# Performance work log

Measured on AMD Instinct MI355X. Metric: run time of the kernel, lower is better.

The kernel has to match this reference:

```python
import jax, jax.numpy as jnp
import numpy as np

B, S, E, H = 2, 2048, 1024, 8
DH = E // H


def setup_inputs() -> dict:
    key = jax.random.key(0)
    ks = jax.random.split(key, 8)
    sc = 1.0 / np.sqrt(E)
    return {
        "q": jax.random.normal(ks[0], (B, S, E), jnp.float32),
        "k": jax.random.normal(ks[1], (B, S, E), jnp.float32),
        "v": jax.random.normal(ks[2], (B, S, E), jnp.float32),
        "Wq": jax.random.normal(ks[3], (E, E), jnp.float32) * sc,
        "bq": jnp.zeros((E,), jnp.float32),
        "Wk": jax.random.normal(ks[4], (E, E), jnp.float32) * sc,
        "bk": jnp.zeros((E,), jnp.float32),
        "Wv": jax.random.normal(ks[5], (E, E), jnp.float32) * sc,
        "bv": jnp.zeros((E,), jnp.float32),
        "Wo": jax.random.normal(ks[6], (E, E), jnp.float32) * sc,
        "bo": jnp.zeros((E,), jnp.float32),
        "is_causal": 1,
    }


def reference(q, k, v, Wq, bq, Wk, bk, Wv, bv, Wo, bo, is_causal):
    # q,k,v: [B,S,E]. Dense projections, split into H heads of dim DH.
    def heads(x, W, b):
        y = x @ W + b                       # [B,S,E]
        return y.reshape(B, S, H, DH).transpose(0, 2, 1, 3)  # [B,H,S,DH]

    qh = heads(q, Wq, bq)
    kh = heads(k, Wk, bk)
    vh = heads(v, Wv, bv)

    scale = 1.0 / jnp.sqrt(jnp.asarray(DH, q.dtype))
    scores = jnp.einsum("bhsd,bhtd->bhst", qh, kh) * scale  # [B,H,S,S]

    if is_causal:
        # tril mask (BigBird layout is all-ones here; causality comes from attn_mask)
        causal = jnp.tril(jnp.ones((S, S), bool))
        neg = jnp.asarray(jnp.finfo(scores.dtype).min, scores.dtype)
        scores = jnp.where(causal[None, None], scores, neg)

    attn = jax.nn.softmax(scores, axis=-1)                  # [B,H,S,S]
    ctx = jnp.einsum("bhst,bhtd->bhsd", attn, vh)           # [B,H,S,DH]
    ctx = ctx.transpose(0, 2, 1, 3).reshape(B, S, E)        # merge heads
    return ctx @ Wo + bo
```

## Files before the change

### kernel.cpp

```cpp
#include <hip/hip_runtime.h>
#include <math.h>


typedef __bf16 bf16_t;
typedef __bf16 bf16x8 __attribute__((ext_vector_type(8)));
typedef float f32x4 __attribute__((ext_vector_type(4)));

#define MFMA16(a, b, c) __builtin_amdgcn_mfma_f32_16x16x32_bf16(a, b, c, 0, 0, 0)

__global__ __launch_bounds__(256) void prep(const float* q, const float* k,
                                            const float* v, bf16_t* qb,
                                            bf16_t* kb, bf16_t* vb,
                                            const float* W0, const float* W1,
                                            const float* W2, const float* W3,
                                            bf16_t* Wt) {
  const int bid = blockIdx.x, tid = threadIdx.x;
  if (bid < 6144) {
    const int z = bid >> 11, chunk = bid & 2047;
    const float* x = (z == 0) ? q : (z == 1) ? k : v;
    bf16_t* y = (z == 0) ? qb : (z == 1) ? kb : vb;
    size_t i = ((size_t)chunk * 256 + tid) * 8;
    float4 a = *(const float4*)(x + i);
    float4 b = *(const float4*)(x + i + 4);
    bf16x8 o = {(bf16_t)a.x, (bf16_t)a.y, (bf16_t)a.z, (bf16_t)a.w,
                (bf16_t)b.x, (bf16_t)b.y, (bf16_t)b.z, (bf16_t)b.w};
    *(bf16x8*)(y + i) = o;
  } else {
    __shared__ float t[32][33];
    const int b2 = bid - 6144;
    const int wz = b2 >> 10, t2 = b2 & 1023;
    const float* W = (wz == 0) ? W0 : (wz == 1) ? W1 : (wz == 2) ? W2 : W3;
    bf16_t* o = Wt + (size_t)wz * 1024 * 1024;
    const int n0 = (t2 & 31) * 32, k0 = (t2 >> 5) * 32;
    const int tx = tid & 31, ty = tid >> 5;
#pragma unroll
    for (int i = 0; i < 4; i++)
      t[ty + 8 * i][tx] = W[(size_t)(k0 + ty + 8 * i) * 1024 + n0 + tx];
    __syncthreads();
#pragma unroll
    for (int i = 0; i < 4; i++)
      o[(size_t)(n0 + ty + 8 * i) * 1024 + k0 + tx] = (bf16_t)t[tx][ty + 8 * i];
  }
}

__global__ __launch_bounds__(256) void gemm_qkv(
    const bf16_t* qb, const bf16_t* kb, const bf16_t* vb, const bf16_t* Wt,
    const float* b0, const float* b1, const float* b2, bf16_t* Qh, bf16_t* Kh,
    bf16_t* Vt) {
  __shared__ bf16_t As[2][128 * 64];
  __shared__ bf16_t Bs[2][128 * 64];
  const int tid = threadIdx.x, w = tid >> 6, lane = tid & 63;
  const int bm = blockIdx.x, bn = blockIdx.y;
  const int wr = w >> 1, wc = w & 1, q4 = lane >> 4, lo = lane & 15;
  const int z = blockIdx.z;
  const bf16_t* A = (z == 0) ? qb : (z == 1) ? kb : vb;
  const bf16_t* Bt = Wt + (size_t)z * 1024 * 1024;
  const float* bias = (z == 0) ? b0 : (z == 1) ? b1 : b2;

  f32x4 acc[4][4];
#pragma unroll
  for (int m = 0; m < 4; m++)
#pragma unroll
    for (int n = 0; n < 4; n++) acc[m][n] = (f32x4){0.f, 0.f, 0.f, 0.f};

  const int r2 = tid >> 1;
  const int cb = (tid & 1) * 4;
  const bf16_t* Arow = A + (size_t)(bm * 128 + r2) * 1024;
  const bf16_t* Brow = Bt + (size_t)(bn * 128 + r2) * 1024;

  bf16x8 ar[4], br[4];
  auto loadAB = [&](int k0) {
#pragma unroll
    for (int i = 0; i < 4; i++) {
      ar[i] = *(const bf16x8*)(Arow + k0 + (cb + i) * 8);
      br[i] = *(const bf16x8*)(Brow + k0 + (cb + i) * 8);
    }
  };

  loadAB(0);
  for (int k = 0; k < 16; k++) {
    const int cur = k & 1;
#pragma unroll
    for (int i = 0; i < 4; i++) {
      *(bf16x8*)&As[cur][r2 * 64 + (((cb + i) ^ (r2 & 7)) * 8)] = ar[i];
      *(bf16x8*)&Bs[cur][r2 * 64 + (((cb + i) ^ (r2 & 7)) * 8)] = br[i];
    }
    if (k < 15) loadAB((k + 1) * 64);
    __syncthreads();

#pragma unroll
    for (int kc = 0; kc < 2; kc++) {
      bf16x8 af[4], bfr[4];
#pragma unroll
      for (int m = 0; m < 4; m++) {
        int rr = wr * 64 + m * 16 + lo;
        af[m] = *(const bf16x8*)&As[cur][rr * 64 + (((kc * 4 + q4) ^ (rr & 7)) * 8)];
      }
#pragma unroll
      for (int n = 0; n < 4; n++) {
        int rr = wc * 64 + n * 16 + lo;
        bfr[n] = *(const bf16x8*)&Bs[cur][rr * 64 + (((kc * 4 + q4) ^ (rr & 7)) * 8)];
      }
#pragma unroll
      for (int m = 0; m < 4; m++)
#pragma unroll
        for (int n = 0; n < 4; n++)
          acc[m][n] = MFMA16(af[m], bfr[n], acc[m][n]);
    }
  }

#pragma unroll
  for (int m = 0; m < 4; m++) {
#pragma unroll
    for (int n = 0; n < 4; n++) {
      int rowg0 = bm * 128 + wr * 64 + m * 16 + q4 * 4;
      int colg = bn * 128 + wc * 64 + n * 16 + lo;
      float bv = bias[colg];
#pragma unroll
      for (int rg = 0; rg < 4; rg++) {
        float val = acc[m][n][rg] + bv;
        int row = rowg0 + rg;
        int b = row >> 11, s = row & 2047;
        int h = colg >> 7, d = colg & 127;
        if (z == 0)
          Qh[(((size_t)(b * 8 + h)) * 2048 + s) * 128 + d] = (bf16_t)val;
        else if (z == 1)
          Kh[(((size_t)(b * 8 + h)) * 2048 + s) * 128 + d] = (bf16_t)val;
        else
          Vt[(((size_t)(b * 8 + h)) * 128 + d) * 2048 + s] = (bf16_t)val;
      }
    }
  }
}

__global__ __launch_bounds__(256) void gemm_out(const bf16_t* ctx,
                                                const bf16_t* Wt3,
                                                const float* bo, float* Of32) {
  __shared__ bf16_t As[2][64 * 64];
  __shared__ bf16_t Bs[2][128 * 64];
  const int tid = threadIdx.x, w = tid >> 6, lane = tid & 63;
  const int bm = blockIdx.x, bn = blockIdx.y;
  const int wr = w >> 1, wc = w & 1, q4 = lane >> 4, lo = lane & 15;

  f32x4 acc[2][4];
#pragma unroll
  for (int m = 0; m < 2; m++)
#pragma unroll
    for (int n = 0; n < 4; n++) acc[m][n] = (f32x4){0.f, 0.f, 0.f, 0.f};

  const int r2a = tid >> 2;
  const int cba = (tid & 3) * 2;
  const int r2b = tid >> 1;
  const int cbb = (tid & 1) * 4;
  const bf16_t* Arow = ctx + (size_t)(bm * 64 + r2a) * 1024;
  const bf16_t* Brow = Wt3 + (size_t)(bn * 128 + r2b) * 1024;

  bf16x8 ar[2], br[4];
  auto loadAB = [&](int k0) {
#pragma unroll
    for (int i = 0; i < 2; i++)
      ar[i] = *(const bf16x8*)(Arow + k0 + (cba + i) * 8);
#pragma unroll
    for (int i = 0; i < 4; i++)
      br[i] = *(const bf16x8*)(Brow + k0 + (cbb + i) * 8);
  };

  loadAB(0);
  for (int k = 0; k < 16; k++) {
    const int cur = k & 1;
#pragma unroll
    for (int i = 0; i < 2; i++)
      *(bf16x8*)&As[cur][r2a * 64 + (((cba + i) ^ (r2a & 7)) * 8)] = ar[i];
#pragma unroll
    for (int i = 0; i < 4; i++)
      *(bf16x8*)&Bs[cur][r2b * 64 + (((cbb + i) ^ (r2b & 7)) * 8)] = br[i];
    if (k < 15) loadAB((k + 1) * 64);
    __syncthreads();

#pragma unroll
    for (int kc = 0; kc < 2; kc++) {
      bf16x8 af[2], bfr[4];
#pragma unroll
      for (int m = 0; m < 2; m++) {
        int rr = wr * 32 + m * 16 + lo;
        af[m] = *(const bf16x8*)&As[cur][rr * 64 + (((kc * 4 + q4) ^ (rr & 7)) * 8)];
      }
#pragma unroll
      for (int n = 0; n < 4; n++) {
        int rr = wc * 64 + n * 16 + lo;
        bfr[n] = *(const bf16x8*)&Bs[cur][rr * 64 + (((kc * 4 + q4) ^ (rr & 7)) * 8)];
      }
#pragma unroll
      for (int m = 0; m < 2; m++)
#pragma unroll
        for (int n = 0; n < 4; n++)
          acc[m][n] = MFMA16(af[m], bfr[n], acc[m][n]);
    }
  }

#pragma unroll
  for (int m = 0; m < 2; m++) {
#pragma unroll
    for (int n = 0; n < 4; n++) {
      int rowg0 = bm * 64 + wr * 32 + m * 16 + q4 * 4;
      int colg = bn * 128 + wc * 64 + n * 16 + lo;
      float bv = bo[colg];
#pragma unroll
      for (int rg = 0; rg < 4; rg++)
        Of32[(size_t)(rowg0 + rg) * 1024 + colg] = acc[m][n][rg] + bv;
    }
  }
}

__global__ __launch_bounds__(256) void flash_k(const bf16_t* Qh,
                                               const bf16_t* Kh,
                                               const bf16_t* Vt, bf16_t* ctx,
                                               const int* causal_p) {
  __shared__ bf16_t sm[32768 + 4 * 1280];
  const int tid = threadIdx.x, w = tid >> 6, lane = tid & 63;
  const int q4 = lane >> 4, lo = lane & 15;
  const int r = w >> 1, kh = w & 1;
  const int n0 = blockIdx.x;
  const int u = n0 & 255, hi = n0 >> 8;
  const int bh = u & 15, p0 = u >> 4;
  const int t = hi ? (31 - p0) : p0;
  const int causal = *causal_p;
  const int kmax = causal ? t : 31;

  bf16_t* Ps = sm + 32768 + w * 1280;

  bf16x8 aq[2][4];
#pragma unroll
  for (int m = 0; m < 2; m++) {
    const bf16_t* qa =
        Qh + ((size_t)bh * 2048 + t * 64 + r * 32 + m * 16 + lo) * 128;
#pragma unroll
    for (int ks = 0; ks < 4; ks++)
      aq[m][ks] = *(const bf16x8*)(qa + ks * 32 + q4 * 8);
  }

  const bf16_t* Kbase = Kh + (size_t)bh * 2048 * 128;
  const bf16_t* Vbase = Vt + (size_t)bh * 128 * 2048;
  const int kr = tid >> 2, kc = (tid & 3) * 4;
  const int vd = tid >> 1, vc = (tid & 1) * 4;

  bf16x8 kreg[4], vreg[4];
  auto loadKV = [&](int kt) {
    const bf16_t* kp = Kbase + (size_t)(kt * 64 + kr) * 128;
    const bf16_t* vp = Vbase + (size_t)vd * 2048 + kt * 64;
#pragma unroll
    for (int i = 0; i < 4; i++) {
      kreg[i] = *(const bf16x8*)(kp + (kc + i) * 8);
      vreg[i] = *(const bf16x8*)(vp + (vc + i) * 8);
    }
  };

  f32x4 acc[2][8];
  f32x4 lacc[2];
#pragma unroll
  for (int m = 0; m < 2; m++) {
#pragma unroll
    for (int i = 0; i < 8; i++) acc[m][i] = (f32x4){0.f, 0.f, 0.f, 0.f};
    lacc[m] = (f32x4){0.f, 0.f, 0.f, 0.f};
  }

  const bf16_t one = (bf16_t)1.0f;
  const bf16x8 vone = {one, one, one, one, one, one, one, one};
  const float sc2 = 0.08838834764831845f * 1.44269504088896f;

  loadKV(0);
  for (int kt = 0; kt <= kmax; ++kt) {
    bf16_t* Kd = sm + (kt & 1) * 8192;
    bf16_t* Vd = sm + 16384 + (kt & 1) * 8192;
#pragma unroll
    for (int i = 0; i < 4; i++)
      *(bf16x8*)&Kd[kr * 128 + (((kc + i) ^ (kr & 7)) * 8)] = kreg[i];
#pragma unroll
    for (int i = 0; i < 4; i++)
      *(bf16x8*)&Vd[vd * 64 + (((vc + i) ^ ((vd >> 1) & 7)) * 8)] = vreg[i];
    if (kt < kmax) loadKV(kt + 1);
    __syncthreads();

    f32x4 sa[2][2];
#pragma unroll
    for (int m = 0; m < 2; m++)
#pragma unroll
      for (int nt = 0; nt < 2; nt++) sa[m][nt] = (f32x4){0.f, 0.f, 0.f, 0.f};
#pragma unroll
    for (int ks = 0; ks < 4; ks++) {
#pragma unroll
      for (int nt = 0; nt < 2; nt++) {
        int key = kh * 32 + nt * 16 + lo;
        bf16x8 bk =
            *(const bf16x8*)&Kd[key * 128 + (((ks * 4 + q4) ^ (key & 7)) * 8)];
        sa[0][nt] = MFMA16(aq[0][ks], bk, sa[0][nt]);
        sa[1][nt] = MFMA16(aq[1][ks], bk, sa[1][nt]);
      }
    }

    const bool diag = causal && (kt == t);
#pragma unroll
    for (int m = 0; m < 2; m++) {
#pragma unroll
      for (int nt = 0; nt < 2; nt++) {
        int keyrel = kh * 32 + nt * 16 + lo;
#pragma unroll
        for (int rg = 0; rg < 4; rg++) {
          int rowrel = r * 32 + m * 16 + q4 * 4 + rg;
          float pv = exp2f(sa[m][nt][rg] * sc2);
          if (diag && keyrel > rowrel) pv = 0.f;
          Ps[(m * 16 + q4 * 4 + rg) * 40 + nt * 16 + lo] = (bf16_t)pv;
        }
      }
    }

    bf16x8 ap[2];
#pragma unroll
    for (int m = 0; m < 2; m++) {
      ap[m] = *(const bf16x8*)&Ps[(m * 16 + lo) * 40 + q4 * 8];
      lacc[m] = MFMA16(ap[m], vone, lacc[m]);
    }
#pragma unroll
    for (int n = 0; n < 8; n++) {
      int d = n * 16 + lo;
      int sw = (d >> 1) & 7;
      bf16x8 bv = *(const bf16x8*)&Vd[d * 64 + (((kh * 4 + q4) ^ sw) * 8)];
      acc[0][n] = MFMA16(ap[0], bv, acc[0][n]);
      acc[1][n] = MFMA16(ap[1], bv, acc[1][n]);
    }
  }

  __syncthreads();
  float* farena = (float*)sm;
  if (kh == 1) {
    int base = r * 4096 + lane * 64;
#pragma unroll
    for (int m = 0; m < 2; m++)
#pragma unroll
      for (int n = 0; n < 8; n++) {
        int c = m * 8 + n;
        *(f32x4*)&farena[base + ((c ^ (lane & 15)) & 15) * 4] = acc[m][n];
      }
    float* lp = (float*)(sm + 32768 + w * 1280);
    *(f32x4*)&lp[lane * 8] = lacc[0];
    *(f32x4*)&lp[lane * 8 + 4] = lacc[1];
  }
  __syncthreads();
  if (kh == 0) {
    int base = r * 4096 + lane * 64;
    float* lp = (float*)(sm + 32768 + (w + 1) * 1280);
    lacc[0] += *(const f32x4*)&lp[lane * 8];
    lacc[1] += *(const f32x4*)&lp[lane * 8 + 4];
#pragma unroll
    for (int m = 0; m < 2; m++)
#pragma unroll
      for (int n = 0; n < 8; n++) {
        int c = m * 8 + n;
        acc[m][n] += *(const f32x4*)&farena[base + ((c ^ (lane & 15)) & 15) * 4];
      }
    int b = bh >> 3, h = bh & 7;
#pragma unroll
    for (int m = 0; m < 2; m++) {
#pragma unroll
      for (int rg = 0; rg < 4; rg++) {
        float inv = 1.f / lacc[m][rg];
        int row = b * 2048 + t * 64 + r * 32 + m * 16 + q4 * 4 + rg;
#pragma unroll
        for (int n = 0; n < 8; n++)
          ctx[(size_t)row * 1024 + h * 128 + n * 16 + lo] =
              (bf16_t)(acc[m][n][rg] * inv);
      }
    }
  }
}

extern "C" void kernel_launch(void* const* d_in, const int* in_sizes, int n_in,
                              void* d_out, int out_size, void* d_ws,
                              size_t ws_size, hipStream_t stream) {
  const float* q = (const float*)d_in[0];
  const float* k = (const float*)d_in[1];
  const float* v = (const float*)d_in[2];
  const float* Wq = (const float*)d_in[3];
  const float* bq = (const float*)d_in[4];
  const float* Wk = (const float*)d_in[5];
  const float* bk = (const float*)d_in[6];
  const float* Wv = (const float*)d_in[7];
  const float* bv = (const float*)d_in[8];
  const float* Wo = (const float*)d_in[9];
  const float* bo = (const float*)d_in[10];
  const int* isc = (const int*)d_in[11];

  char* ws = (char*)d_ws;
  bf16_t* Wt = (bf16_t*)ws;
  bf16_t* qb = (bf16_t*)(ws + (8ull << 20));
  bf16_t* kb = (bf16_t*)(ws + (16ull << 20));
  bf16_t* vb = (bf16_t*)(ws + (24ull << 20));
  bf16_t* Qh = (bf16_t*)(ws + (32ull << 20));
  bf16_t* Kh = (bf16_t*)(ws + (40ull << 20));
  bf16_t* Vt = (bf16_t*)(ws + (48ull << 20));
  bf16_t* ctx = (bf16_t*)(ws + (8ull << 20));

  prep<<<dim3(10240), 256, 0, stream>>>(q, k, v, qb, kb, vb, Wq, Wk, Wv, Wo, Wt);

  gemm_qkv<<<dim3(32, 8, 3), 256, 0, stream>>>(qb, kb, vb, Wt, bq, bk, bv, Qh,
                                               Kh, Vt);

  flash_k<<<dim3(512), 256, 0, stream>>>(Qh, Kh, Vt, ctx, isc);

  gemm_out<<<dim3(64, 8), 256, 0, stream>>>(ctx, Wt + 3ull * 1024 * 1024, bo,
                                            (float*)d_out);
}
```

Before: 221.2 us.

## Split flash attention across 8 waves and load V directly into registers

Doubles the flash-attention block to 512 threads so each wave owns 16 query rows instead of 32, halving per-wave accumulator registers and raising occupancy. V is no longer staged through shared memory; each lane loads its V fragments straight from global memory in MFMA operand layout, which frees LDS and removes the V store and swizzle. The trade-off is uncoalesced strided global reads of V per iteration with no prefetch, and K tiles are now shared by twice as many waves.

```diff
diff --git a/kernel.cpp b/kernel.cpp
--- a/kernel.cpp
+++ b/kernel.cpp
@@ -212,11 +212,11 @@
   }
 }
 
-__global__ __launch_bounds__(256) void flash_k(const bf16_t* Qh,
-                                               const bf16_t* Kh,
-                                               const bf16_t* Vt, bf16_t* ctx,
-                                               const int* causal_p) {
-  __shared__ bf16_t sm[32768 + 4 * 1280];
+__global__ __launch_bounds__(512, 4) void flash_k(const bf16_t* Qh,
+                                                  const bf16_t* Kh,
+                                                  const bf16_t* Vt, bf16_t* ctx,
+                                                  const int* causal_p) {
+  __shared__ bf16_t sm[16384 + 8 * 640];
   const int tid = threadIdx.x, w = tid >> 6, lane = tid & 63;
   const int q4 = lane >> 4, lo = lane & 15;
   const int r = w >> 1, kh = w & 1;
@@ -227,65 +227,55 @@
   const int causal = *causal_p;
   const int kmax = causal ? t : 31;
 
-  bf16_t* Ps = sm + 32768 + w * 1280;
-
-  bf16x8 aq[2][4];
-#pragma unroll
-  for (int m = 0; m < 2; m++) {
+  bf16_t* Ps = sm + 16384 + w * 640;
+
+  bf16x8 aq[4];
+  {
     const bf16_t* qa =
-        Qh + ((size_t)bh * 2048 + t * 64 + r * 32 + m * 16 + lo) * 128;
+        Qh + ((size_t)bh * 2048 + t * 64 + r * 16 + lo) * 128;
 #pragma unroll
     for (int ks = 0; ks < 4; ks++)
-      aq[m][ks] = *(const bf16x8*)(qa + ks * 32 + q4 * 8);
+      aq[ks] = *(const bf16x8*)(qa + ks * 32 + q4 * 8);
   }
 
   const bf16_t* Kbase = Kh + (size_t)bh * 2048 * 128;
-  const bf16_t* Vbase = Vt + (size_t)bh * 128 * 2048;
-  const int kr = tid >> 2, kc = (tid & 3) * 4;
-  const int vd = tid >> 1, vc = (tid & 1) * 4;
-
-  bf16x8 kreg[4], vreg[4];
-  auto loadKV = [&](int kt) {
+  const bf16_t* Vb = Vt + ((size_t)bh * 128 + lo) * 2048 + kh * 32 + q4 * 8;
+  const int kr = tid >> 3, kc = (tid & 7) * 2;
+
+  bf16x8 kreg[2], vreg[8];
+  auto loadK = [&](int kt) {
     const bf16_t* kp = Kbase + (size_t)(kt * 64 + kr) * 128;
-    const bf16_t* vp = Vbase + (size_t)vd * 2048 + kt * 64;
-#pragma unroll
-    for (int i = 0; i < 4; i++) {
-      kreg[i] = *(const bf16x8*)(kp + (kc + i) * 8);
-      vreg[i] = *(const bf16x8*)(vp + (vc + i) * 8);
-    }
+#pragma unroll
+    for (int i = 0; i < 2; i++) kreg[i] = *(const bf16x8*)(kp + (kc + i) * 8);
   };
-
-  f32x4 acc[2][8];
-  f32x4 lacc[2];
-#pragma unroll
-  for (int m = 0; m < 2; m++) {
-#pragma unroll
-    for (int i = 0; i < 8; i++) acc[m][i] = (f32x4){0.f, 0.f, 0.f, 0.f};
-    lacc[m] = (f32x4){0.f, 0.f, 0.f, 0.f};
-  }
+  auto loadV = [&](int kt) {
+#pragma unroll
+    for (int n = 0; n < 8; n++)
+      vreg[n] = *(const bf16x8*)(Vb + (size_t)n * (16 * 2048) + kt * 64);
+  };
+
+  f32x4 acc[8], lacc;
+#pragma unroll
+  for (int i = 0; i < 8; i++) acc[i] = (f32x4){0.f, 0.f, 0.f, 0.f};
+  lacc = (f32x4){0.f, 0.f, 0.f, 0.f};
 
   const bf16_t one = (bf16_t)1.0f;
   const bf16x8 vone = {one, one, one, one, one, one, one, one};
   const float sc2 = 0.08838834764831845f * 1.44269504088896f;
 
-  loadKV(0);
+  loadK(0);
   for (int kt = 0; kt <= kmax; ++kt) {
     bf16_t* Kd = sm + (kt & 1) * 8192;
-    bf16_t* Vd = sm + 16384 + (kt & 1) * 8192;
-#pragma unroll
-    for (int i = 0; i < 4; i++)
+#pragma unroll
+    for (int i = 0; i < 2; i++)
       *(bf16x8*)&Kd[kr * 128 + (((kc + i) ^ (kr & 7)) * 8)] = kreg[i];
-#pragma unroll
-    for (int i = 0; i < 4; i++)
-      *(bf16x8*)&Vd[vd * 64 + (((vc + i) ^ ((vd >> 1) & 7)) * 8)] = vreg[i];
-    if (kt < kmax) loadKV(kt + 1);
+    if (kt < kmax) loadK(kt + 1);
+    loadV(kt);
     __syncthreads();
 
-    f32x4 sa[2][2];
-#pragma unroll
-    for (int m = 0; m < 2; m++)
-#pragma unroll
-      for (int nt = 0; nt < 2; nt++) sa[m][nt] = (f32x4){0.f, 0.f, 0.f, 0.f};
+    f32x4 sa[2];
+#pragma unroll
+    for (int nt = 0; nt < 2; nt++) sa[nt] = (f32x4){0.f, 0.f, 0.f, 0.f};
 #pragma unroll
     for (int ks = 0; ks < 4; ks++) {
 #pragma unroll
@@ -293,83 +283,56 @@
         int key = kh * 32 + nt * 16 + lo;
         bf16x8 bk =
             *(const bf16x8*)&Kd[key * 128 + (((ks * 4 + q4) ^ (key & 7)) * 8)];
-        sa[0][nt] = MFMA16(aq[0][ks], bk, sa[0][nt]);
-        sa[1][nt] = MFMA16(aq[1][ks], bk, sa[1][nt]);
+        sa[nt] = MFMA16(aq[ks], bk, sa[nt]);
       }
     }
 
     const bool diag = causal && (kt == t);
 #pragma unroll
-    for (int m = 0; m < 2; m++) {
-#pragma unroll
-      for (int nt = 0; nt < 2; nt++) {
-        int keyrel = kh * 32 + nt * 16 + lo;
-#pragma unroll
-        for (int rg = 0; rg < 4; rg++) {
-          int rowrel = r * 32 + m * 16 + q4 * 4 + rg;
-          float pv = exp2f(sa[m][nt][rg] * sc2);
-          if (diag && keyrel > rowrel) pv = 0.f;
-          Ps[(m * 16 + q4 * 4 + rg) * 40 + nt * 16 + lo] = (bf16_t)pv;
-        }
-      }
-    }
-
-    bf16x8 ap[2];
-#pragma unroll
-    for (int m = 0; m < 2; m++) {
-      ap[m] = *(const bf16x8*)&Ps[(m * 16 + lo) * 40 + q4 * 8];
-      lacc[m] = MFMA16(ap[m], vone, lacc[m]);
-    }
-#pragma unroll
-    for (int n = 0; n < 8; n++) {
-      int d = n * 16 + lo;
-      int sw = (d >> 1) & 7;
-      bf16x8 bv = *(const bf16x8*)&Vd[d * 64 + (((kh * 4 + q4) ^ sw) * 8)];
-      acc[0][n] = MFMA16(ap[0], bv, acc[0][n]);
-      acc[1][n] = MFMA16(ap[1], bv, acc[1][n]);
-    }
+    for (int nt = 0; nt < 2; nt++) {
+      int keyrel = kh * 32 + nt * 16 + lo;
+#pragma unroll
+      for (int rg = 0; rg < 4; rg++) {
+        int rowrel = r * 16 + q4 * 4 + rg;
+        float pv = exp2f(sa[nt][rg] * sc2);
+        if (diag && keyrel > rowrel) pv = 0.f;
+        Ps[(q4 * 4 + rg) * 40 + nt * 16 + lo] = (bf16_t)pv;
+      }
+    }
+
+    bf16x8 ap = *(const bf16x8*)&Ps[lo * 40 + q4 * 8];
+    lacc = MFMA16(ap, vone, lacc);
+#pragma unroll
+    for (int n = 0; n < 8; n++) acc[n] = MFMA16(ap, vreg[n], acc[n]);
   }
 
   __syncthreads();
   float* farena = (float*)sm;
   if (kh == 1) {
-    int base = r * 4096 + lane * 64;
-#pragma unroll
-    for (int m = 0; m < 2; m++)
-#pragma unroll
-      for (int n = 0; n < 8; n++) {
-        int c = m * 8 + n;
-        *(f32x4*)&farena[base + ((c ^ (lane & 15)) & 15) * 4] = acc[m][n];
-      }
-    float* lp = (float*)(sm + 32768 + w * 1280);
-    *(f32x4*)&lp[lane * 8] = lacc[0];
-    *(f32x4*)&lp[lane * 8 + 4] = lacc[1];
+    int base = r * 2048 + lane * 32;
+#pragma unroll
+    for (int n = 0; n < 8; n++)
+      *(f32x4*)&farena[base + ((n ^ (lane & 7)) & 7) * 4] = acc[n];
+    float* lp = (float*)(sm + 16384 + w * 640);
+    *(f32x4*)&lp[lane * 4] = lacc;
   }
   __syncthreads();
   if (kh == 0) {
-    int base = r * 4096 + lane * 64;
-    float* lp = (float*)(sm + 32768 + (w + 1) * 1280);
-    lacc[0] += *(const f32x4*)&lp[lane * 8];
-    lacc[1] += *(const f32x4*)&lp[lane * 8 + 4];
-#pragma unroll
-    for (int m = 0; m < 2; m++)
-#pragma unroll
-      for (int n = 0; n < 8; n++) {
-        int c = m * 8 + n;
-        acc[m][n] += *(const f32x4*)&farena[base + ((c ^ (lane & 15)) & 15) * 4];
-      }
+    int base = r * 2048 + lane * 32;
+    float* lp = (float*)(sm + 16384 + (w + 1) * 640);
+    lacc += *(const f32x4*)&lp[lane * 4];
+#pragma unroll
+    for (int n = 0; n < 8; n++)
+      acc[n] += *(const f32x4*)&farena[base + ((n ^ (lane & 7)) & 7) * 4];
     int b = bh >> 3, h = bh & 7;
 #pragma unroll
-    for (int m = 0; m < 2; m++) {
-#pragma unroll
-      for (int rg = 0; rg < 4; rg++) {
-        float inv = 1.f / lacc[m][rg];
-        int row = b * 2048 + t * 64 + r * 32 + m * 16 + q4 * 4 + rg;
-#pragma unroll
-        for (int n = 0; n < 8; n++)
-          ctx[(size_t)row * 1024 + h * 128 + n * 16 + lo] =
-              (bf16_t)(acc[m][n][rg] * inv);
-      }
+    for (int rg = 0; rg < 4; rg++) {
+      float inv = 1.f / lacc[rg];
+      int row = b * 2048 + t * 64 + r * 16 + q4 * 4 + rg;
+#pragma unroll
+      for (int n = 0; n < 8; n++)
+        ctx[(size_t)row * 1024 + h * 128 + n * 16 + lo] =
+            (bf16_t)(acc[n][rg] * inv);
     }
   }
 }
@@ -405,7 +368,7 @@
   gemm_qkv<<<dim3(32, 8, 3), 256, 0, stream>>>(qb, kb, vb, Wt, bq, bk, bv, Qh,
                                                Kh, Vt);
 
-  flash_k<<<dim3(512), 256, 0, stream>>>(Qh, Kh, Vt, ctx, isc);
+  flash_k<<<dim3(512), 512, 0, stream>>>(Qh, Kh, Vt, ctx, isc);
 
   gemm_out<<<dim3(64, 8), 256, 0, stream>>>(ctx, Wt + 3ull * 1024 * 1024, bo,
                                             (float*)d_out);
```

Result: slower. 242.7 us (+9.7%).
